# Optimization experiments

Measured on AMD Instinct MI355X. Metric: run time of the kernel, lower is better.

Reference implementation:

```python
import jax, jax.numpy as jnp
import numpy as np

TOP_K = 2
NORM_MIN = 1e-12
B, S, H = 2, 1024, 2048
E, I = 16, 1024
SHARED_I = 2048  # moe_intermediate_size * moe_num_shared_experts


def setup_inputs() -> dict:
    key = jax.random.key(0)
    ks = jax.random.split(key, 8)
    s = 0.02  # init scale
    return {
        "hidden_states": jax.random.normal(ks[0], (B, S, H), jnp.float32),
        "router_w": jax.random.normal(ks[1], (E, H), jnp.float32) * s,
        "w_gate": jax.random.normal(ks[2], (E, H, I), jnp.float32) * s,
        "w_up": jax.random.normal(ks[3], (E, H, I), jnp.float32) * s,
        "w_down": jax.random.normal(ks[4], (E, I, H), jnp.float32) * s,
        "ws_gate": jax.random.normal(ks[5], (H, SHARED_I), jnp.float32) * s,
        "ws_up": jax.random.normal(ks[6], (H, SHARED_I), jnp.float32) * s,
        "ws_down": jax.random.normal(ks[7], (SHARED_I, H), jnp.float32) * s,
    }


def reference(hidden_states, router_w, w_gate, w_up, w_down, ws_gate, ws_up, ws_down):
    b, s, h = hidden_states.shape
    x = hidden_states.reshape(-1, h)                      # [N, H]
    n = x.shape[0]

    # Router: float32 softmax -> top-k -> renormalize with clamp
    router_logits = x.astype(jnp.float32) @ router_w.T    # [N, E]
    probs = jax.nn.softmax(router_logits, axis=-1)
    rw, sel = jax.lax.top_k(probs, TOP_K)                 # [N, K]
    rw = rw / jnp.clip(rw.sum(axis=-1, keepdims=True), NORM_MIN)
    rw = rw.astype(x.dtype)

    # Dense combine weights [N, E] (equivalent to one_hot dispatch/scatter)
    combine = jnp.zeros((n, E), x.dtype).at[jnp.arange(n)[:, None], sel].set(rw)

    # All-expert SwiGLU MLP (full-capacity MoE, no dropped tokens)
    g = jnp.einsum('nh,ehi->eni', x, w_gate)              # [E, N, I]
    u = jnp.einsum('nh,ehi->eni', x, w_up)
    o = jnp.einsum('eni,eih->enh', jax.nn.silu(g) * u, w_down)  # [E, N, H]
    out = jnp.einsum('enh,ne->nh', o, combine)            # weighted combine

    # Shared expert path
    shared = (jax.nn.silu(x @ ws_gate) * (x @ ws_up)) @ ws_down
    out = out + shared

    return out.reshape(b, s, h), router_logits
```

## Files before the change

kernel.cpp:

```cpp
#include <hip/hip_runtime.h>
#include <cstdint>
#include <cstddef>
#include <cmath>

#define N_TOK 2048
#define HDIM  2048
#define NEXP  16
#define IDIM  1024
#define SIDIM 2048
#define NTHREADS 256

typedef __attribute__((ext_vector_type(8))) short bf16x8;
typedef __attribute__((ext_vector_type(4))) float f32x4;

__device__ __forceinline__ uint32_t f2bf_u(float f) {
    union { float f; uint32_t u; } v; v.f = f;
    return (v.u + 0x7FFFu + ((v.u >> 16) & 1u)) >> 16;
}

__device__ __forceinline__ uint32_t cvtpk(float lo, float hi) {
    uint32_t r;
    asm("v_cvt_pk_bf16_f32 %0, %1, %2" : "=v"(r) : "v"(lo), "v"(hi));
    return r;
}

__device__ __forceinline__ int swz(int row, int c) {
    return row * 4 + (c ^ ((row >> 1) & 3));
}

__global__ __launch_bounds__(NTHREADS)
void convert_x_kernel(const float* __restrict__ x, unsigned short* __restrict__ xb)
{
    const size_t i = ((size_t)blockIdx.x * NTHREADS + threadIdx.x) * 8;
    float4 a = *(const float4*)(x + i);
    float4 b = *(const float4*)(x + i + 4);
    uint4 w = make_uint4(cvtpk(a.x, a.y), cvtpk(a.z, a.w),
                         cvtpk(b.x, b.y), cvtpk(b.z, b.w));
    *(uint4*)(xb + i) = w;
}

__global__ __launch_bounds__(NTHREADS)
void router_kernel(const float* __restrict__ x,
                   const float* __restrict__ rw,
                   float* __restrict__ logits_out,
                   int* __restrict__ cnt,
                   int* __restrict__ tok_list,
                   float* __restrict__ wt_list)
{
    const int n = blockIdx.x;
    const int tid = threadIdx.x;
    const float* xr = x + (size_t)n * HDIM;

    float acc[NEXP];
#pragma unroll
    for (int e = 0; e < NEXP; ++e) acc[e] = 0.f;

    for (int h = tid; h < HDIM; h += NTHREADS) {
        float xv = xr[h];
#pragma unroll
        for (int e = 0; e < NEXP; ++e) acc[e] += xv * rw[(size_t)e * HDIM + h];
    }

    __shared__ float red[NEXP][NTHREADS];
#pragma unroll
    for (int e = 0; e < NEXP; ++e) red[e][tid] = acc[e];
    __syncthreads();
    for (int s = NTHREADS / 2; s > 0; s >>= 1) {
        if (tid < s) {
#pragma unroll
            for (int e = 0; e < NEXP; ++e) red[e][tid] += red[e][tid + s];
        }
        __syncthreads();
    }

    if (tid < NEXP) logits_out[(size_t)n * NEXP + tid] = red[tid][0];

    if (tid == 0) {
        float l[NEXP];
#pragma unroll
        for (int e = 0; e < NEXP; ++e) l[e] = red[e][0];
        int e0 = 0;
#pragma unroll
        for (int e = 1; e < NEXP; ++e) if (l[e] > l[e0]) e0 = e;
        int e1 = (e0 == 0) ? 1 : 0;
#pragma unroll
        for (int e = 0; e < NEXP; ++e)
            if (e != e0 && l[e] > l[e1]) e1 = e;
        float t = expf(l[e1] - l[e0]);
        float s = 1.f + t;
        float rw0 = 1.f / s;
        float rw1 = t / s;
        int p0 = atomicAdd(&cnt[e0], 1);
        tok_list[e0 * N_TOK + p0] = n;
        wt_list[e0 * N_TOK + p0] = rw0;
        int p1 = atomicAdd(&cnt[e1], 1);
        tok_list[e1 * N_TOK + p1] = n;
        wt_list[e1 * N_TOK + p1] = rw1;
    }
}

__global__ void prefix_kernel(const int* __restrict__ cnt, int* __restrict__ base)
{
    if (threadIdx.x == 0) {
        int s = 0;
        for (int e = 0; e < NEXP; ++e) { base[e] = s; s += cnt[e]; }
    }
}

__global__ __launch_bounds__(NTHREADS)
void dual_swiglu_mfma(const unsigned short* __restrict__ Xb,
                      const float* __restrict__ WgAll,
                      const float* __restrict__ WuAll,
                      const float* __restrict__ Wsg,
                      const float* __restrict__ Wsu,
                      unsigned short* __restrict__ Ysparse,
                      unsigned short* __restrict__ Yshared,
                      const int* __restrict__ cnt,
                      const int* __restrict__ base,
                      const int* __restrict__ tok_list)
{
    const int z  = blockIdx.z;
    const bool shared_path = (z == 0);
    const int e  = z - 1;
    const int Icols = shared_path ? SIDIM : IDIM;
    const int m0 = blockIdx.y * 128;
    const int n0 = blockIdx.x * 64;
    if (n0 >= Icols) return;
    const int M = shared_path ? N_TOK : cnt[e];
    if (m0 >= M) return;
    const float* Wg = shared_path ? Wsg : WgAll + (size_t)e * HDIM * IDIM;
    const float* Wu = shared_path ? Wsu : WuAll + (size_t)e * HDIM * IDIM;
    unsigned short* Y = shared_path ? Yshared : Ysparse;
    const int yb = shared_path ? 0 : base[e];

    __shared__ short As[128 * 32];
    __shared__ short Gs[64 * 32];
    __shared__ short Us[64 * 32];

    const int tid  = threadIdx.x;
    const int lane = tid & 63;
    const int wave = tid >> 6;
    const int wm   = wave >> 1;
    const int wn   = wave & 1;
    const int l15  = lane & 15;
    const int q    = lane >> 4;

    const int ar = tid >> 1;
    const int at = tid & 1;
    const int slotA = m0 + ar;
    int xrow;
    if (!shared_path) xrow = tok_list[e * N_TOK + ((slotA < M) ? slotA : (M - 1))];
    else              xrow = slotA;
    const unsigned short* xp = Xb + (size_t)xrow * HDIM + at * 16;

    const int wcn = tid & 63;
    const int wcc = tid >> 6;
    const float* gp = Wg + n0 + wcn;
    const float* up = Wu + n0 + wcn;

    f32x4 accg[4][2], accu[4][2];
#pragma unroll
    for (int i = 0; i < 4; ++i)
#pragma unroll
        for (int j = 0; j < 2; ++j) {
            accg[i][j] = (f32x4){0.f, 0.f, 0.f, 0.f};
            accu[i][j] = (f32x4){0.f, 0.f, 0.f, 0.f};
        }

    uint4 a0, a1;
    float g8[8], u8[8];
    auto ldtile = [&](int kk) {
        a0 = *(const uint4*)(xp + kk);
        a1 = *(const uint4*)(xp + kk + 8);
#pragma unroll
        for (int j = 0; j < 8; ++j) {
            g8[j] = gp[(size_t)(kk + wcc * 8 + j) * Icols];
            u8[j] = up[(size_t)(kk + wcc * 8 + j) * Icols];
        }
    };

    ldtile(0);
    for (int k0 = 0; k0 < HDIM; k0 += 32) {
        __syncthreads();
        *(uint4*)(As + swz(ar, at * 2 + 0) * 8) = a0;
        *(uint4*)(As + swz(ar, at * 2 + 1) * 8) = a1;
        uint4 gw = make_uint4(cvtpk(g8[0], g8[1]), cvtpk(g8[2], g8[3]),
                              cvtpk(g8[4], g8[5]), cvtpk(g8[6], g8[7]));
        uint4 uw = make_uint4(cvtpk(u8[0], u8[1]), cvtpk(u8[2], u8[3]),
                              cvtpk(u8[4], u8[5]), cvtpk(u8[6], u8[7]));
        *(uint4*)(Gs + swz(wcn, wcc) * 8) = gw;
        *(uint4*)(Us + swz(wcn, wcc) * 8) = uw;
        __syncthreads();

        int kn = k0 + 32;
        if (kn >= HDIM) kn = k0;
        ldtile(kn);

        bf16x8 af[4], bg[2], bu[2];
#pragma unroll
        for (int i = 0; i < 4; ++i)
            af[i] = *(const bf16x8*)(As + swz(wm * 64 + i * 16 + l15, q) * 8);
#pragma unroll
        for (int j = 0; j < 2; ++j) {
            bg[j] = *(const bf16x8*)(Gs + swz(wn * 32 + j * 16 + l15, q) * 8);
            bu[j] = *(const bf16x8*)(Us + swz(wn * 32 + j * 16 + l15, q) * 8);
        }
#pragma unroll
        for (int i = 0; i < 4; ++i)
#pragma unroll
            for (int j = 0; j < 2; ++j) {
                accg[i][j] = __builtin_amdgcn_mfma_f32_16x16x32_bf16(af[i], bg[j], accg[i][j], 0, 0, 0);
                accu[i][j] = __builtin_amdgcn_mfma_f32_16x16x32_bf16(af[i], bu[j], accu[i][j], 0, 0, 0);
            }
    }

#pragma unroll
    for (int i = 0; i < 4; ++i) {
#pragma unroll
        for (int r = 0; r < 4; ++r) {
            const int slot = m0 + wm * 64 + i * 16 + q * 4 + r;
            if (slot < M) {
                unsigned short* yrow = Y + (size_t)(yb + slot) * Icols;
#pragma unroll
                for (int j = 0; j < 2; ++j) {
                    const int col = n0 + wn * 32 + j * 16 + l15;
                    float g = accg[i][j][r];
                    float u = accu[i][j][r];
                    float y = (g / (1.f + expf(-g))) * u;
                    yrow[col] = (unsigned short)f2bf_u(y);
                }
            }
        }
    }
}

__global__ __launch_bounds__(NTHREADS)
void down_mfma(const unsigned short* __restrict__ Ash,
               const unsigned short* __restrict__ Asp,
               const float* __restrict__ Wsd,
               const float* __restrict__ WdAll,
               float* __restrict__ out,
               const int* __restrict__ cnt,
               const int* __restrict__ base,
               const int* __restrict__ tok_list,
               const float* __restrict__ wt_list)
{
    const int z  = blockIdx.z;
    const bool shared_path = (z == 0);
    const int e  = z - 1;
    const int K  = shared_path ? SIDIM : IDIM;
    const int m0 = blockIdx.y * 64;
    const int n0 = blockIdx.x * 128;
    const int M = shared_path ? N_TOK : cnt[e];
    if (m0 >= M) return;
    const unsigned short* A = shared_path ? Ash : Asp;
    const float* Wd = shared_path ? Wsd : WdAll + (size_t)e * IDIM * HDIM;
    const int yb = shared_path ? 0 : base[e];

    __shared__ short As[64 * 32];
    __shared__ short Bs[128 * 32];

    const int tid  = threadIdx.x;
    const int lane = tid & 63;
    const int wave = tid >> 6;
    const int wm   = wave >> 1;
    const int wn   = wave & 1;
    const int l15  = lane & 15;
    const int q    = lane >> 4;

    const int ar = tid >> 2;
    const int ac = tid & 3;
    const int slotA = m0 + ar;
    const int arow = yb + ((slotA < M) ? slotA : (M - 1));
    const unsigned short* ap = A + (size_t)arow * K + ac * 8;

    const int bn = tid & 127;
    const int bh = tid >> 7;
    const float* bp = Wd + n0 + bn;

    f32x4 acc[2][4];
#pragma unroll
    for (int i = 0; i < 2; ++i)
#pragma unroll
        for (int j = 0; j < 4; ++j) acc[i][j] = (f32x4){0.f, 0.f, 0.f, 0.f};

    uint4 a0;
    float b16[16];
    auto ldtile = [&](int kk) {
        a0 = *(const uint4*)(ap + kk);
#pragma unroll
        for (int c = 0; c < 2; ++c)
#pragma unroll
            for (int j = 0; j < 8; ++j)
                b16[c * 8 + j] = bp[(size_t)(kk + (bh * 2 + c) * 8 + j) * HDIM];
    };

    ldtile(0);
    for (int k0 = 0; k0 < K; k0 += 32) {
        __syncthreads();
        *(uint4*)(As + swz(ar, ac) * 8) = a0;
        uint4 w0 = make_uint4(cvtpk(b16[0], b16[1]),  cvtpk(b16[2], b16[3]),
                              cvtpk(b16[4], b16[5]),  cvtpk(b16[6], b16[7]));
        uint4 w1 = make_uint4(cvtpk(b16[8], b16[9]),  cvtpk(b16[10], b16[11]),
                              cvtpk(b16[12], b16[13]), cvtpk(b16[14], b16[15]));
        *(uint4*)(Bs + swz(bn, bh * 2 + 0) * 8) = w0;
        *(uint4*)(Bs + swz(bn, bh * 2 + 1) * 8) = w1;
        __syncthreads();

        int kn = k0 + 32;
        if (kn >= K) kn = k0;
        ldtile(kn);

        bf16x8 af[2], bfr[4];
#pragma unroll
        for (int i = 0; i < 2; ++i)
            af[i] = *(const bf16x8*)(As + swz(wm * 32 + i * 16 + l15, q) * 8);
#pragma unroll
        for (int j = 0; j < 4; ++j)
            bfr[j] = *(const bf16x8*)(Bs + swz(wn * 64 + j * 16 + l15, q) * 8);
#pragma unroll
        for (int i = 0; i < 2; ++i)
#pragma unroll
            for (int j = 0; j < 4; ++j)
                acc[i][j] = __builtin_amdgcn_mfma_f32_16x16x32_bf16(af[i], bfr[j], acc[i][j], 0, 0, 0);
    }

#pragma unroll
    for (int i = 0; i < 2; ++i) {
#pragma unroll
        for (int r = 0; r < 4; ++r) {
            const int slot = m0 + wm * 32 + i * 16 + q * 4 + r;
            if (slot >= M) continue;
            const int tok  = shared_path ? slot : tok_list[e * N_TOK + slot];
            const float wt = shared_path ? 1.f  : wt_list[e * N_TOK + slot];
            float* orow = out + (size_t)tok * HDIM;
#pragma unroll
            for (int j = 0; j < 4; ++j) {
                const int col = n0 + wn * 64 + j * 16 + l15;
                atomicAdd(&orow[col], wt * acc[i][j][r]);
            }
        }
    }
}

extern "C" void kernel_launch(void* const* d_in, const int* in_sizes, int n_in,
                              void* d_out, int out_size, void* d_ws, size_t ws_size,
                              hipStream_t stream)
{
    const float* x       = (const float*)d_in[0];
    const float* rw      = (const float*)d_in[1];
    const float* w_gate  = (const float*)d_in[2];
    const float* w_up    = (const float*)d_in[3];
    const float* w_down  = (const float*)d_in[4];
    const float* ws_gate = (const float*)d_in[5];
    const float* ws_up   = (const float*)d_in[6];
    const float* ws_down = (const float*)d_in[7];

    float* out    = (float*)d_out;
    float* logits = out + (size_t)N_TOK * HDIM;

    char* w = (char*)d_ws;
    int* cnt      = (int*)w;
    int* base     = cnt + 16;
    int* tok_list = base + 16;
    float* wt_list = (float*)(tok_list + NEXP * N_TOK);
    uintptr_t p = (uintptr_t)(wt_list + NEXP * N_TOK);
    p = (p + 255) & ~(uintptr_t)255;
    unsigned short* Xb       = (unsigned short*)p;
    unsigned short* A_shared = Xb + (size_t)N_TOK * HDIM;
    unsigned short* Ybuf     = A_shared + (size_t)N_TOK * SIDIM;

    hipMemsetAsync(cnt, 0, 16 * sizeof(int), stream);
    hipMemsetAsync(out, 0, (size_t)N_TOK * HDIM * sizeof(float), stream);

    convert_x_kernel<<<dim3((N_TOK * HDIM) / (NTHREADS * 8)), dim3(NTHREADS), 0, stream>>>(x, Xb);
    router_kernel<<<dim3(N_TOK), dim3(NTHREADS), 0, stream>>>(
        x, rw, logits, cnt, tok_list, wt_list);
    prefix_kernel<<<dim3(1), dim3(64), 0, stream>>>(cnt, base);

    dual_swiglu_mfma<<<dim3(SIDIM / 64, N_TOK / 128, NEXP + 1), dim3(NTHREADS), 0, stream>>>(
        Xb, w_gate, w_up, ws_gate, ws_up, Ybuf, A_shared, cnt, base, tok_list);

    down_mfma<<<dim3(HDIM / 128, N_TOK / 64, NEXP + 1), dim3(NTHREADS), 0, stream>>>(
        A_shared, Ybuf, ws_down, w_down, out, cnt, base, tok_list, wt_list);
}
```

Baseline: 756.4 us.

## Pre-transpose weights to bf16 and stream GEMM tiles via direct global-to-LDS loads

```diff
diff --git a/kernel.cpp b/kernel.cpp
--- a/kernel.cpp
+++ b/kernel.cpp
@@ -24,6 +24,12 @@
     return r;
 }
 
+__device__ __forceinline__ void gload_lds16(const void* g, void* l) {
+    __builtin_amdgcn_global_load_lds(
+        (const __attribute__((address_space(1))) uint32_t*)g,
+        (__attribute__((address_space(3))) uint32_t*)l, 16, 0, 0);
+}
+
 __device__ __forceinline__ int swz(int row, int c) {
     return row * 4 + (c ^ ((row >> 1) & 3));
 }
@@ -37,6 +43,45 @@
     uint4 w = make_uint4(cvtpk(a.x, a.y), cvtpk(a.z, a.w),
                          cvtpk(b.x, b.y), cvtpk(b.z, b.w));
     *(uint4*)(xb + i) = w;
+}
+
+#define TP 68
+__global__ __launch_bounds__(NTHREADS)
+void transpose_w(const float* __restrict__ src, unsigned short* __restrict__ dst,
+                 const int K, const int N)
+{
+    const size_t moff = (size_t)blockIdx.z * K * N;
+    src += moff; dst += moff;
+    const int k0 = blockIdx.y * 64;
+    const int n0 = blockIdx.x * 64;
+    __shared__ short t[64 * TP];
+    const int tid = threadIdx.x;
+
+    {
+        const int c  = tid & 15;
+        const int r0 = (tid >> 4) * 4;
+#pragma unroll
+        for (int it = 0; it < 4; ++it) {
+            const int r = r0 + it;
+            float4 v = *(const float4*)(src + (size_t)(k0 + r) * N + n0 + c * 4);
+            uint2 p; p.x = cvtpk(v.x, v.y); p.y = cvtpk(v.z, v.w);
+            *(uint2*)(&t[r * TP + c * 4]) = p;
+        }
+    }
+    __syncthreads();
+
+    {
+        const int c2  = tid & 7;
+        const int nr0 = tid >> 3;
+#pragma unroll
+        for (int it = 0; it < 2; ++it) {
+            const int n = nr0 + it * 32;
+            union { unsigned short v[8]; uint4 u4; } tmp;
+#pragma unroll
+            for (int j = 0; j < 8; ++j) tmp.v[j] = (unsigned short)t[(c2 * 8 + j) * TP + n];
+            *(uint4*)(dst + (size_t)(n0 + n) * K + k0 + c2 * 8) = tmp.u4;
+        }
+    }
 }
 
 __global__ __launch_bounds__(NTHREADS)
@@ -107,17 +152,274 @@
     }
 }
 
+
 __global__ __launch_bounds__(NTHREADS)
-void dual_swiglu_mfma(const unsigned short* __restrict__ Xb,
-                      const float* __restrict__ WgAll,
-                      const float* __restrict__ WuAll,
-                      const float* __restrict__ Wsg,
-                      const float* __restrict__ Wsu,
-                      unsigned short* __restrict__ Ysparse,
-                      unsigned short* __restrict__ Yshared,
-                      const int* __restrict__ cnt,
-                      const int* __restrict__ base,
-                      const int* __restrict__ tok_list)
+void dual_swiglu_gl(const unsigned short* __restrict__ Xb,
+                    const unsigned short* __restrict__ WgT,
+                    const unsigned short* __restrict__ WuT,
+                    const unsigned short* __restrict__ WsgT,
+                    const unsigned short* __restrict__ WsuT,
+                    unsigned short* __restrict__ Ysparse,
+                    unsigned short* __restrict__ Yshared,
+                    const int* __restrict__ cnt,
+                    const int* __restrict__ base,
+                    const int* __restrict__ tok_list)
+{
+    const int z = blockIdx.z;
+    const bool shared_path = (z == 0);
+    const int e = z - 1;
+    const int Icols = shared_path ? SIDIM : IDIM;
+    const int m0 = blockIdx.y * 128;
+    const int n0 = blockIdx.x * 64;
+    if (n0 >= Icols) return;
+    const int M = shared_path ? N_TOK : cnt[e];
+    if (m0 >= M) return;
+    const unsigned short* Wg = shared_path ? WsgT : WgT + (size_t)e * IDIM * HDIM;
+    const unsigned short* Wu = shared_path ? WsuT : WuT + (size_t)e * IDIM * HDIM;
+    unsigned short* Y = shared_path ? Yshared : Ysparse;
+    const int yb = shared_path ? 0 : base[e];
+
+    __shared__ short As[2][128 * 64];
+    __shared__ short Gs[2][64 * 64];
+    __shared__ short Us[2][64 * 64];
+
+    const int tid  = threadIdx.x;
+    const int lane = tid & 63;
+    const int w    = tid >> 6;
+    const int wm   = w >> 1;
+    const int wn   = w & 1;
+    const int l15  = lane & 15;
+    const int q    = lane >> 4;
+    const int lr   = lane >> 3;
+    const int cl   = (lane & 7) ^ lr;
+
+    const unsigned short* aSrc[4];
+#pragma unroll
+    for (int i = 0; i < 4; ++i) {
+        const int row  = (w * 4 + i) * 8 + lr;
+        const int slot = m0 + row;
+        const int xrow = shared_path ? slot
+                       : tok_list[e * N_TOK + (slot < M ? slot : M - 1)];
+        aSrc[i] = Xb + (size_t)xrow * HDIM + cl * 8;
+    }
+    const unsigned short *gSrc[2], *uSrc[2];
+#pragma unroll
+    for (int i = 0; i < 2; ++i) {
+        const int n = (w * 2 + i) * 8 + lr;
+        gSrc[i] = Wg + (size_t)(n0 + n) * HDIM + cl * 8;
+        uSrc[i] = Wu + (size_t)(n0 + n) * HDIM + cl * 8;
+    }
+
+    f32x4 accg[4][2], accu[4][2];
+#pragma unroll
+    for (int i = 0; i < 4; ++i)
+#pragma unroll
+        for (int j = 0; j < 2; ++j) {
+            accg[i][j] = (f32x4){0.f, 0.f, 0.f, 0.f};
+            accu[i][j] = (f32x4){0.f, 0.f, 0.f, 0.f};
+        }
+
+    auto stage = [&](int b, int k0) {
+#pragma unroll
+        for (int i = 0; i < 4; ++i)
+            gload_lds16(aSrc[i] + k0, &As[b][(w * 4 + i) * 512]);
+#pragma unroll
+        for (int i = 0; i < 2; ++i) {
+            gload_lds16(gSrc[i] + k0, &Gs[b][(w * 2 + i) * 512]);
+            gload_lds16(uSrc[i] + k0, &Us[b][(w * 2 + i) * 512]);
+        }
+    };
+    auto compute = [&](int b) {
+#pragma unroll
+        for (int kk = 0; kk < 2; ++kk) {
+            bf16x8 af[4], bg[2], bu[2];
+#pragma unroll
+            for (int i = 0; i < 4; ++i) {
+                const int row = wm * 64 + i * 16 + l15;
+                const int c = (q + kk * 4) ^ (row & 7);
+                af[i] = *(const bf16x8*)(&As[b][row * 64 + c * 8]);
+            }
+#pragma unroll
+            for (int j = 0; j < 2; ++j) {
+                const int row = wn * 32 + j * 16 + l15;
+                const int c = (q + kk * 4) ^ (row & 7);
+                bg[j] = *(const bf16x8*)(&Gs[b][row * 64 + c * 8]);
+                bu[j] = *(const bf16x8*)(&Us[b][row * 64 + c * 8]);
+            }
+#pragma unroll
+            for (int i = 0; i < 4; ++i)
+#pragma unroll
+                for (int j = 0; j < 2; ++j) {
+                    accg[i][j] = __builtin_amdgcn_mfma_f32_16x16x32_bf16(af[i], bg[j], accg[i][j], 0, 0, 0);
+                    accu[i][j] = __builtin_amdgcn_mfma_f32_16x16x32_bf16(af[i], bu[j], accu[i][j], 0, 0, 0);
+                }
+        }
+    };
+
+    stage(0, 0);
+    asm volatile("s_waitcnt vmcnt(0)" ::: "memory");
+    __builtin_amdgcn_s_barrier();
+    int cur = 0;
+    const int NT = HDIM / 64;
+    for (int t = 0; t < NT; ++t) {
+        if (t + 1 < NT) stage(cur ^ 1, (t + 1) * 64);
+        compute(cur);
+        asm volatile("s_waitcnt vmcnt(0)" ::: "memory");
+        __builtin_amdgcn_s_barrier();
+        cur ^= 1;
+    }
+
+#pragma unroll
+    for (int i = 0; i < 4; ++i) {
+#pragma unroll
+        for (int r = 0; r < 4; ++r) {
+            const int slot = m0 + wm * 64 + i * 16 + q * 4 + r;
+            if (slot < M) {
+                unsigned short* yrow = Y + (size_t)(yb + slot) * Icols;
+#pragma unroll
+                for (int j = 0; j < 2; ++j) {
+                    const int col = n0 + wn * 32 + j * 16 + l15;
+                    float g = accg[i][j][r];
+                    float u = accu[i][j][r];
+                    float y = (g / (1.f + expf(-g))) * u;
+                    yrow[col] = (unsigned short)f2bf_u(y);
+                }
+            }
+        }
+    }
+}
+
+__global__ __launch_bounds__(NTHREADS)
+void down_gl(const unsigned short* __restrict__ Ash,
+             const unsigned short* __restrict__ Asp,
+             const unsigned short* __restrict__ WsdT,
+             const unsigned short* __restrict__ WdT,
+             float* __restrict__ out,
+             const int* __restrict__ cnt,
+             const int* __restrict__ base,
+             const int* __restrict__ tok_list,
+             const float* __restrict__ wt_list)
+{
+    const int z = blockIdx.z;
+    const bool shared_path = (z == 0);
+    const int e = z - 1;
+    const int K = shared_path ? SIDIM : IDIM;
+    const int m0 = blockIdx.y * 64;
+    const int n0 = blockIdx.x * 128;
+    const int M = shared_path ? N_TOK : cnt[e];
+    if (m0 >= M) return;
+    const unsigned short* A  = shared_path ? Ash : Asp;
+    const unsigned short* WT = shared_path ? WsdT : WdT + (size_t)e * HDIM * IDIM;
+    const int yb = shared_path ? 0 : base[e];
+
+    __shared__ short As_[2][64 * 64];
+    __shared__ short Bs_[2][128 * 64];
+
+    const int tid  = threadIdx.x;
+    const int lane = tid & 63;
+    const int w    = tid >> 6;
+    const int wm   = w >> 1;
+    const int wn   = w & 1;
+    const int l15  = lane & 15;
+    const int q    = lane >> 4;
+    const int lr   = lane >> 3;
+    const int cl   = (lane & 7) ^ lr;
+
+    const unsigned short* aSrc[2];
+#pragma unroll
+    for (int i = 0; i < 2; ++i) {
+        const int row  = (w * 2 + i) * 8 + lr;
+        const int slot = m0 + row;
+        const int arow = yb + (slot < M ? slot : M - 1);
+        aSrc[i] = A + (size_t)arow * K + cl * 8;
+    }
+    const unsigned short* bSrc[4];
+#pragma unroll
+    for (int i = 0; i < 4; ++i) {
+        const int n = (w * 4 + i) * 8 + lr;
+        bSrc[i] = WT + (size_t)(n0 + n) * K + cl * 8;
+    }
+
+    f32x4 acc[2][4];
+#pragma unroll
+    for (int i = 0; i < 2; ++i)
+#pragma unroll
+        for (int j = 0; j < 4; ++j) acc[i][j] = (f32x4){0.f, 0.f, 0.f, 0.f};
+
+    auto stage = [&](int b, int k0) {
+#pragma unroll
+        for (int i = 0; i < 2; ++i)
+            gload_lds16(aSrc[i] + k0, &As_[b][(w * 2 + i) * 512]);
+#pragma unroll
+        for (int i = 0; i < 4; ++i)
+            gload_lds16(bSrc[i] + k0, &Bs_[b][(w * 4 + i) * 512]);
+    };
+    auto compute = [&](int b) {
+#pragma unroll
+        for (int kk = 0; kk < 2; ++kk) {
+            bf16x8 af[2], bf[4];
+#pragma unroll
+            for (int i = 0; i < 2; ++i) {
+                const int row = wm * 32 + i * 16 + l15;
+                const int c = (q + kk * 4) ^ (row & 7);
+                af[i] = *(const bf16x8*)(&As_[b][row * 64 + c * 8]);
+            }
+#pragma unroll
+            for (int j = 0; j < 4; ++j) {
+                const int row = wn * 64 + j * 16 + l15;
+                const int c = (q + kk * 4) ^ (row & 7);
+                bf[j] = *(const bf16x8*)(&Bs_[b][row * 64 + c * 8]);
+            }
+#pragma unroll
+            for (int i = 0; i < 2; ++i)
+#pragma unroll
+                for (int j = 0; j < 4; ++j)
+                    acc[i][j] = __builtin_amdgcn_mfma_f32_16x16x32_bf16(af[i], bf[j], acc[i][j], 0, 0, 0);
+        }
+    };
+
+    stage(0, 0);
+    asm volatile("s_waitcnt vmcnt(0)" ::: "memory");
+    __builtin_amdgcn_s_barrier();
+    int cur = 0;
+    const int NT = K / 64;
+    for (int t = 0; t < NT; ++t) {
+        if (t + 1 < NT) stage(cur ^ 1, (t + 1) * 64);
+        compute(cur);
+        asm volatile("s_waitcnt vmcnt(0)" ::: "memory");
+        __builtin_amdgcn_s_barrier();
+        cur ^= 1;
+    }
+
+#pragma unroll
+    for (int i = 0; i < 2; ++i) {
+#pragma unroll
+        for (int r = 0; r < 4; ++r) {
+            const int slot = m0 + wm * 32 + i * 16 + q * 4 + r;
+            if (slot >= M) continue;
+            const int tok  = shared_path ? slot : tok_list[e * N_TOK + slot];
+            const float wt = shared_path ? 1.f  : wt_list[e * N_TOK + slot];
+            float* orow = out + (size_t)tok * HDIM;
+#pragma unroll
+            for (int j = 0; j < 4; ++j) {
+                const int col = n0 + wn * 64 + j * 16 + l15;
+                atomicAdd(&orow[col], wt * acc[i][j][r]);
+            }
+        }
+    }
+}
+
+__global__ __launch_bounds__(NTHREADS)
+void dual_swiglu_fb(const unsigned short* __restrict__ Xb,
+                    const float* __restrict__ WgAll,
+                    const float* __restrict__ WuAll,
+                    const float* __restrict__ Wsg,
+                    const float* __restrict__ Wsu,
+                    unsigned short* __restrict__ Ysparse,
+                    unsigned short* __restrict__ Yshared,
+                    const int* __restrict__ cnt,
+                    const int* __restrict__ base,
+                    const int* __restrict__ tok_list)
 {
     const int z  = blockIdx.z;
     const bool shared_path = (z == 0);
@@ -235,15 +537,15 @@
 }
 
 __global__ __launch_bounds__(NTHREADS)
-void down_mfma(const unsigned short* __restrict__ Ash,
-               const unsigned short* __restrict__ Asp,
-               const float* __restrict__ Wsd,
-               const float* __restrict__ WdAll,
-               float* __restrict__ out,
-               const int* __restrict__ cnt,
-               const int* __restrict__ base,
-               const int* __restrict__ tok_list,
-               const float* __restrict__ wt_list)
+void down_fb(const unsigned short* __restrict__ Ash,
+             const unsigned short* __restrict__ Asp,
+             const float* __restrict__ Wsd,
+             const float* __restrict__ WdAll,
+             float* __restrict__ out,
+             const int* __restrict__ cnt,
+             const int* __restrict__ base,
+             const int* __restrict__ tok_list,
+             const float* __restrict__ wt_list)
 {
     const int z  = blockIdx.z;
     const bool shared_path = (z == 0);
@@ -369,6 +671,13 @@
     unsigned short* Xb       = (unsigned short*)p;
     unsigned short* A_shared = Xb + (size_t)N_TOK * HDIM;
     unsigned short* Ybuf     = A_shared + (size_t)N_TOK * SIDIM;
+    unsigned short* WgT      = Ybuf + (size_t)2 * N_TOK * IDIM;
+    unsigned short* WuT      = WgT + (size_t)NEXP * IDIM * HDIM;
+    unsigned short* WdT      = WuT + (size_t)NEXP * IDIM * HDIM;
+    unsigned short* WsgT     = WdT + (size_t)NEXP * HDIM * IDIM;
+    unsigned short* WsuT     = WsgT + (size_t)SIDIM * HDIM;
+    unsigned short* WsdT     = WsuT + (size_t)SIDIM * HDIM;
+    const size_t need = (size_t)((char*)(WsdT + (size_t)HDIM * SIDIM) - (char*)d_ws);
 
     hipMemsetAsync(cnt, 0, 16 * sizeof(int), stream);
     hipMemsetAsync(out, 0, (size_t)N_TOK * HDIM * sizeof(float), stream);
@@ -378,9 +687,28 @@
         x, rw, logits, cnt, tok_list, wt_list);
     prefix_kernel<<<dim3(1), dim3(64), 0, stream>>>(cnt, base);
 
-    dual_swiglu_mfma<<<dim3(SIDIM / 64, N_TOK / 128, NEXP + 1), dim3(NTHREADS), 0, stream>>>(
-        Xb, w_gate, w_up, ws_gate, ws_up, Ybuf, A_shared, cnt, base, tok_list);
-
-    down_mfma<<<dim3(HDIM / 128, N_TOK / 64, NEXP + 1), dim3(NTHREADS), 0, stream>>>(
-        A_shared, Ybuf, ws_down, w_down, out, cnt, base, tok_list, wt_list);
-}
+    if (ws_size >= need) {
+        transpose_w<<<dim3(IDIM / 64, HDIM / 64, NEXP), dim3(NTHREADS), 0, stream>>>(
+            w_gate, WgT, HDIM, IDIM);
+        transpose_w<<<dim3(IDIM / 64, HDIM / 64, NEXP), dim3(NTHREADS), 0, stream>>>(
+            w_up, WuT, HDIM, IDIM);
+        transpose_w<<<dim3(HDIM / 64, IDIM / 64, NEXP), dim3(NTHREADS), 0, stream>>>(
+            w_down, WdT, IDIM, HDIM);
+        transpose_w<<<dim3(SIDIM / 64, HDIM / 64, 1), dim3(NTHREADS), 0, stream>>>(
+            ws_gate, WsgT, HDIM, SIDIM);
+        transpose_w<<<dim3(SIDIM / 64, HDIM / 64, 1), dim3(NTHREADS), 0, stream>>>(
+            ws_up, WsuT, HDIM, SIDIM);
+        transpose_w<<<dim3(HDIM / 64, SIDIM / 64, 1), dim3(NTHREADS), 0, stream>>>(
+            ws_down, WsdT, SIDIM, HDIM);
+
+        dual_swiglu_gl<<<dim3(SIDIM / 64, N_TOK / 128, NEXP + 1), dim3(NTHREADS), 0, stream>>>(
+            Xb, WgT, WuT, WsgT, WsuT, Ybuf, A_shared, cnt, base, tok_list);
+        down_gl<<<dim3(HDIM / 128, N_TOK / 64, NEXP + 1), dim3(NTHREADS), 0, stream>>>(
+            A_shared, Ybuf, WsdT, WdT, out, cnt, base, tok_list, wt_list);
+    } else {
+        dual_swiglu_fb<<<dim3(SIDIM / 64, N_TOK / 128, NEXP + 1), dim3(NTHREADS), 0, stream>>>(
+            Xb, w_gate, w_up, ws_gate, ws_up, Ybuf, A_shared, cnt, base, tok_list);
+        down_fb<<<dim3(HDIM / 128, N_TOK / 64, NEXP + 1), dim3(NTHREADS), 0, stream>>>(
+            A_shared, Ybuf, ws_down, w_down, out, cnt, base, tok_list, wt_list);
+    }
+}
```

After: 777.2 us. +2.7%, slower.
